# Optimization experiments

Measured on AMD Instinct MI355X. Metric: run time of the kernel, lower is better.

Reference implementation:

```python
import jax, jax.numpy as jnp
import numpy as np

B, T, OUT, IN, H = 128, 512, 256, 1024, 1024  # batch, seq_len, output_size, hidden_size(lstm in), input_size(lstm hidden)


def lstm_layer(x_seq, Wih, Whh, bih, bhh):
    """Single LSTM layer, PyTorch gate order (i, f, g, o).
    x_seq: [B, T, In] -> h_seq: [B, T, H]"""
    # input contribution is independent of the recurrence: compute once
    gx = jnp.einsum('bti,gi->btg', x_seq, Wih) + bih  # [B, T, 4H]
    gx = jnp.swapaxes(gx, 0, 1)  # [T, B, 4H] for scan over time
    Hh = Whh.shape[1]

    def step(carry, gxt):
        h, c = carry
        gates = gxt + h @ Whh.T + bhh  # [B, 4H]
        i, f, g, o = jnp.split(gates, 4, axis=-1)
        i = jax.nn.sigmoid(i)
        f = jax.nn.sigmoid(f)
        g = jnp.tanh(g)
        o = jax.nn.sigmoid(o)
        c = f * c + i * g
        h = o * jnp.tanh(c)
        return (h, c), h

    h0 = jnp.zeros((x_seq.shape[0], Hh), dtype=x_seq.dtype)
    c0 = jnp.zeros_like(h0)
    _, hs = jax.lax.scan(step, (h0, c0), gx)
    return jnp.swapaxes(hs, 0, 1)  # [B, T, H]


def setup_inputs() -> dict:
    key = jax.random.key(0)
    ks = jax.random.split(key, 12)
    s_fc = 1.0 / np.sqrt(OUT)
    s_l = 1.0 / np.sqrt(H)
    inp = {
        'x': jax.random.normal(ks[0], (B, OUT), dtype=jnp.float32),
        'fc_w': jax.random.uniform(ks[1], (IN, OUT), jnp.float32, -s_fc, s_fc),
        'fc_b': jax.random.uniform(ks[2], (IN,), jnp.float32, -s_fc, s_fc),
        'Wih0': jax.random.uniform(ks[3], (4 * H, IN), jnp.float32, -s_l, s_l),
        'Whh0': jax.random.uniform(ks[4], (4 * H, H), jnp.float32, -s_l, s_l),
        'bih0': jax.random.uniform(ks[5], (4 * H,), jnp.float32, -s_l, s_l),
        'bhh0': jax.random.uniform(ks[6], (4 * H,), jnp.float32, -s_l, s_l),
        'Wih1': jax.random.uniform(ks[7], (4 * H, H), jnp.float32, -s_l, s_l),
        'Whh1': jax.random.uniform(ks[8], (4 * H, H), jnp.float32, -s_l, s_l),
        'bih1': jax.random.uniform(ks[9], (4 * H,), jnp.float32, -s_l, s_l),
        'bhh1': jax.random.uniform(ks[10], (4 * H,), jnp.float32, -s_l, s_l),
    }
    return inp


def reference(x, fc_w, fc_b, Wih0, Whh0, bih0, bhh0, Wih1, Whh1, bih1, bhh1):
    # fc + (eval-mode) dropout, then broadcast the constant input across time
    z = x @ fc_w.T + fc_b  # [B, IN]
    z_seq = jnp.broadcast_to(z[:, None, :], (z.shape[0], T, z.shape[1]))  # [B, T, IN]
    h1 = lstm_layer(z_seq, Wih0, Whh0, bih0, bhh0)  # [B, T, H]
    # inter-layer dropout is identity in eval mode
    h2 = lstm_layer(h1, Wih1, Whh1, bih1, bhh1)  # [B, T, H]
    return h2
```

## Files before the change

kernel.cpp:

```cpp
#include <hip/hip_runtime.h>

typedef __attribute__((ext_vector_type(8))) short bf16x8;
typedef __attribute__((ext_vector_type(4))) float f32x4;
typedef unsigned short u16;
typedef unsigned long long u64;

#define T_SEQ 512
#define NBLK  192
#define FPAD  16
#define RSLOT 4

__device__ __forceinline__ u16 f2bf(float f) {
  unsigned int u = __float_as_uint(f);
  u += 0x7fffu + ((u >> 16) & 1u);
  return (u16)(u >> 16);
}
__device__ __forceinline__ float sigm_(float x) { return 1.f / (1.f + __expf(-x)); }
__device__ __forceinline__ float tanh_(float x) { return 1.f - 2.f / (__expf(2.f * x) + 1.f); }

template <typename T>
__device__ __forceinline__ void st_agent(T* p, T v) {
  __hip_atomic_store(p, v, __ATOMIC_RELAXED, __HIP_MEMORY_SCOPE_AGENT);
}
template <typename T>
__device__ __forceinline__ T ld_agent(const T* p) {
  return __hip_atomic_load(p, __ATOMIC_RELAXED, __HIP_MEMORY_SCOPE_AGENT);
}
__device__ __forceinline__ u64 pack2f(float a, float b) {
  return (u64)__float_as_uint(a) | ((u64)__float_as_uint(b) << 32);
}
__device__ __forceinline__ u64 pack4bf(f32x4 v) {
  return (u64)f2bf(v[0]) | ((u64)f2bf(v[1]) << 16) |
         ((u64)f2bf(v[2]) << 32) | ((u64)f2bf(v[3]) << 48);
}

__global__ void fc_kernel(const float* __restrict__ x, const float* __restrict__ w,
                          const float* __restrict__ bias, float* __restrict__ z) {
  int idx = blockIdx.x * 256 + threadIdx.x;
  int b = idx >> 10, i = idx & 1023;
  const float* xr = x + b * 256;
  const float* wr = w + i * 256;
  float acc = bias[i];
  #pragma unroll 4
  for (int o = 0; o < 256; ++o) acc += xr[o] * wr[o];
  z[idx] = acc;
}

__global__ void gx0_kernel(const float* __restrict__ z, const float* __restrict__ Wih0,
                           const float* __restrict__ bih, const float* __restrict__ bhh,
                           float* __restrict__ gx0) {
  int idx = blockIdx.x * 256 + threadIdx.x;
  int b = idx >> 12, j = idx & 4095;
  const float* zr = z + b * 1024;
  const float* wr = Wih0 + (size_t)j * 1024;
  float acc = bih[j] + bhh[j];
  #pragma unroll 4
  for (int k = 0; k < 1024; ++k) acc += zr[k] * wr[k];
  gx0[idx] = acc;
}

__global__ __launch_bounds__(512, 2)
void lstm_persist(const float* __restrict__ Whh0, const float* __restrict__ Wih1,
                  const float* __restrict__ Whh1, const float* __restrict__ gx0,
                  const float* __restrict__ bih1, const float* __restrict__ bhh1,
                  u16* __restrict__ h0ring, u16* __restrict__ h1ring,
                  float* __restrict__ pabuf, float* __restrict__ out,
                  int* __restrict__ h0flag, int* __restrict__ paflag,
                  int* __restrict__ h1flag) {
  __shared__ __align__(16) u16 wlds[4][2048][8];
  __shared__ __align__(16) float red[4][64][20];
  __shared__ __align__(16) float stage[128][20];

  const int bid = blockIdx.x;
  const int role = bid >> 6;
  const int cslice = bid & 63;
  const int cb = cslice * 16;
  const int tid = threadIdx.x;
  const int w = tid >> 6;
  const int lane = tid & 63;
  const int l15 = lane & 15;
  const int q = lane >> 4;
  const int Mg = w & 3;
  const int kh = w >> 2;

  {
    const float* Wsrc = (role == 0) ? Whh0 : (role == 1) ? Wih1 : Whh1;
    const int r = tid >> 3;
    const int g = r >> 4, n = r & 15;
    const int k0 = (tid & 7) * 128;
    const float* src = Wsrc + (((size_t)(g * 1024 + cb + n)) << 10) + k0;
    for (int k = 0; k < 128; k += 4) {
      float4 v = *(const float4*)(src + k);
      ushort4 o;
      o.x = f2bf(v.x); o.y = f2bf(v.y); o.z = f2bf(v.z); o.w = f2bf(v.w);
      const int kk = k0 + k;
      *(ushort4*)&wlds[g][((kk >> 3) << 4) + n][kk & 7] = o;
    }
  }

  float c_st[2][4];
  #pragma unroll
  for (int mt = 0; mt < 2; ++mt)
    #pragma unroll
    for (int r = 0; r < 4; ++r) c_st[mt][r] = 0.f;

  float gx[2][4][4];
  float b1[4];
  if (role == 0 && w < 4) {
    #pragma unroll
    for (int mt = 0; mt < 2; ++mt)
      #pragma unroll
      for (int g = 0; g < 4; ++g)
        #pragma unroll
        for (int r = 0; r < 4; ++r)
          gx[mt][g][r] = gx0[(size_t)(w * 32 + mt * 16 + q * 4 + r) * 4096 + g * 1024 + cb + l15];
  }
  if (role == 2 && w < 4) {
    #pragma unroll
    for (int g = 0; g < 4; ++g)
      b1[g] = bih1[g * 1024 + cb + l15] + bhh1[g * 1024 + cb + l15];
  }
  __syncthreads();

  const size_t HSLOT = (size_t)128 * 1024;

  for (int t = 0; t < T_SEQ; ++t) {
    const int sA = (t + 3) & 3;
    const int sW = t & 3;

    if (w == 0) {
      bool ok;
      if (role == 0) {
        do {
          int fa = ld_agent(h0flag + (sA * 64 + lane) * FPAD);
          int fb = ld_agent(paflag + (sW * 64 + lane) * FPAD);
          ok = __all(fa >= t && fb >= t - 3);
          if (!ok) __builtin_amdgcn_s_sleep(1);
        } while (!ok);
      } else if (role == 1) {
        do {
          int fa = ld_agent(h0flag + (sW * 64 + lane) * FPAD);
          int fb = (lane == 0) ? ld_agent(h1flag + (sW * 64 + cslice) * FPAD)
                               : 0x7fffffff;
          ok = __all(fa >= t + 1 && fb >= t - 3);
          if (!ok) __builtin_amdgcn_s_sleep(1);
        } while (!ok);
      } else {
        do {
          int fa = ld_agent(h1flag + (sA * 64 + lane) * FPAD);
          int fb = (lane == 0) ? ld_agent(paflag + (sW * 64 + cslice) * FPAD)
                               : 0x7fffffff;
          ok = __all(fa >= t && fb >= t + 1);
          if (!ok) __builtin_amdgcn_s_sleep(1);
        } while (!ok);
      }
      __builtin_amdgcn_fence(__ATOMIC_ACQUIRE, "agent");
    }
    __syncthreads();

    const u16* A = (role == 0) ? h0ring + (size_t)sA * HSLOT
                 : (role == 1) ? h0ring + (size_t)sW * HSLOT
                               : h1ring + (size_t)sA * HSLOT;

    const int kbase = kh * 512;
    const u16* Ap = A + (((size_t)(Mg * 32 + l15)) << 10) + kbase + q * 8;
    const int cellbase = ((kbase >> 3) + q) * 16 + l15;

    f32x4 acc0[4] = {{0.f,0.f,0.f,0.f},{0.f,0.f,0.f,0.f},{0.f,0.f,0.f,0.f},{0.f,0.f,0.f,0.f}};
    f32x4 acc1[4] = {{0.f,0.f,0.f,0.f},{0.f,0.f,0.f,0.f},{0.f,0.f,0.f,0.f},{0.f,0.f,0.f,0.f}};

    #pragma unroll
    for (int kk = 0; kk < 16; ++kk) {
      bf16x8 a0 = *(const bf16x8*)(Ap + kk * 32);
      bf16x8 a1 = *(const bf16x8*)(Ap + (16 << 10) + kk * 32);
      #pragma unroll
      for (int g = 0; g < 4; ++g) {
        bf16x8 b = *(const bf16x8*)&wlds[g][cellbase + kk * 64][0];
        acc0[g] = __builtin_amdgcn_mfma_f32_16x16x32_bf16(a0, b, acc0[g], 0, 0, 0);
        acc1[g] = __builtin_amdgcn_mfma_f32_16x16x32_bf16(a1, b, acc1[g], 0, 0, 0);
      }
    }

    u64 pa64[16];
    const float* pr = pabuf + (size_t)sW * 524288 + (size_t)(cslice * 4 + w) * 2048;
    if (role == 2 && w < 4) {
      #pragma unroll
      for (int j = 0; j < 8; ++j) {
        pa64[j * 2]     = ld_agent((const u64*)pr + j * 128 + lane * 2);
        pa64[j * 2 + 1] = ld_agent((const u64*)pr + j * 128 + lane * 2 + 1);
      }
    }

    if (w >= 4) {
      #pragma unroll
      for (int g = 0; g < 4; ++g) *(f32x4*)&red[w - 4][lane][g * 4] = acc0[g];
    }
    __syncthreads();
    if (w < 4) {
      #pragma unroll
      for (int g = 0; g < 4; ++g) acc0[g] += *(const f32x4*)&red[w][lane][g * 4];
    }
    __syncthreads();
    if (w >= 4) {
      #pragma unroll
      for (int g = 0; g < 4; ++g) *(f32x4*)&red[w - 4][lane][g * 4] = acc1[g];
    }
    __syncthreads();
    if (w < 4) {
      #pragma unroll
      for (int g = 0; g < 4; ++g) acc1[g] += *(const f32x4*)&red[w][lane][g * 4];

      if (role == 1) {
        float* pw = pabuf + (size_t)sW * 524288 + (size_t)(cslice * 4 + w) * 2048;
        #pragma unroll
        for (int g = 0; g < 4; ++g) {
          st_agent((u64*)pw + g * 128 + lane * 2,           pack2f(acc0[g][0], acc0[g][1]));
          st_agent((u64*)pw + g * 128 + lane * 2 + 1,       pack2f(acc0[g][2], acc0[g][3]));
          st_agent((u64*)pw + (4 + g) * 128 + lane * 2,     pack2f(acc1[g][0], acc1[g][1]));
          st_agent((u64*)pw + (4 + g) * 128 + lane * 2 + 1, pack2f(acc1[g][2], acc1[g][3]));
        }
      } else {
        #pragma unroll
        for (int mt = 0; mt < 2; ++mt) {
          #pragma unroll
          for (int r = 0; r < 4; ++r) {
            float xi, xf, xg, xo;
            f32x4* a = mt ? acc1 : acc0;
            if (role == 0) {
              xi = a[0][r] + gx[mt][0][r];
              xf = a[1][r] + gx[mt][1][r];
              xg = a[2][r] + gx[mt][2][r];
              xo = a[3][r] + gx[mt][3][r];
            } else {
              const int h2 = r >> 1, lo = r & 1;
              auto up = [&](int j) {
                u64 v = pa64[j * 2 + h2];
                return __uint_as_float(lo ? (unsigned)(v >> 32) : (unsigned)v);
              };
              xi = a[0][r] + up(mt * 4 + 0) + b1[0];
              xf = a[1][r] + up(mt * 4 + 1) + b1[1];
              xg = a[2][r] + up(mt * 4 + 2) + b1[2];
              xo = a[3][r] + up(mt * 4 + 3) + b1[3];
            }
            float i_ = sigm_(xi), f_ = sigm_(xf), g_ = tanh_(xg), o_ = sigm_(xo);
            float cn = f_ * c_st[mt][r] + i_ * g_;
            c_st[mt][r] = cn;
            float h = o_ * tanh_(cn);
            stage[w * 32 + mt * 16 + q * 4 + r][l15] = h;
          }
        }
      }
    }

    if (role != 1) {
      __syncthreads();
      const int row = tid >> 2, qt = tid & 3;
      f32x4 v = *(const f32x4*)&stage[row][qt * 4];
      u64 pk = pack4bf(v);
      if (role == 0) {
        st_agent((u64*)(h0ring + (size_t)sW * HSLOT + ((size_t)row << 10) + cb) + qt, pk);
      } else {
        st_agent((u64*)(h1ring + (size_t)sW * HSLOT + ((size_t)row << 10) + cb) + qt, pk);
        *(f32x4*)(out + (size_t)row * ((size_t)T_SEQ * 1024) + (size_t)t * 1024 + cb + qt * 4) = v;
      }
    }

    __syncthreads();
    if (tid == 0) {
      if (role == 0)      st_agent(h0flag + (sW * 64 + cslice) * FPAD, t + 1);
      else if (role == 1) st_agent(paflag + (sW * 64 + cslice) * FPAD, t + 1);
      else                st_agent(h1flag + (sW * 64 + cslice) * FPAD, t + 1);
    }
  }
}

extern "C" void kernel_launch(void* const* d_in, const int* in_sizes, int n_in,
                              void* d_out, int out_size, void* d_ws, size_t ws_size,
                              hipStream_t stream) {
  (void)in_sizes; (void)n_in; (void)out_size; (void)ws_size;
  const float* x    = (const float*)d_in[0];
  const float* fc_w = (const float*)d_in[1];
  const float* fc_b = (const float*)d_in[2];
  const float* Wih0 = (const float*)d_in[3];
  const float* Whh0 = (const float*)d_in[4];
  const float* bih0 = (const float*)d_in[5];
  const float* bhh0 = (const float*)d_in[6];
  const float* Wih1 = (const float*)d_in[7];
  const float* Whh1 = (const float*)d_in[8];
  const float* bih1 = (const float*)d_in[9];
  const float* bhh1 = (const float*)d_in[10];
  float* out = (float*)d_out;

  char* ws = (char*)d_ws;
  size_t off = 0;
  auto alloc = [&](size_t bytes) -> void* {
    void* p = ws + off;
    off += (bytes + 255) & ~(size_t)255;
    return p;
  };
  float* z      = (float*)alloc((size_t)128 * 1024 * 4);
  float* gx0    = (float*)alloc((size_t)128 * 4096 * 4);
  u16*   h0ring = (u16*)alloc((size_t)RSLOT * 128 * 1024 * 2);
  u16*   h1ring = (u16*)alloc((size_t)RSLOT * 128 * 1024 * 2);
  float* pabuf  = (float*)alloc((size_t)RSLOT * 524288 * 4);
  int*   h0flag = (int*)alloc((size_t)RSLOT * 64 * FPAD * 4);
  int*   paflag = (int*)alloc((size_t)RSLOT * 64 * FPAD * 4);
  int*   h1flag = (int*)alloc((size_t)RSLOT * 64 * FPAD * 4);

  hipMemsetAsync(h0ring, 0, (size_t)RSLOT * 128 * 1024 * 2, stream);
  hipMemsetAsync(h1ring, 0, (size_t)RSLOT * 128 * 1024 * 2, stream);
  hipMemsetAsync(h0flag, 0, (size_t)RSLOT * 64 * FPAD * 4, stream);
  hipMemsetAsync(paflag, 0, (size_t)RSLOT * 64 * FPAD * 4, stream);
  hipMemsetAsync(h1flag, 0, (size_t)RSLOT * 64 * FPAD * 4, stream);

  fc_kernel<<<512, 256, 0, stream>>>(x, fc_w, fc_b, z);
  gx0_kernel<<<2048, 256, 0, stream>>>(z, Wih0, bih0, bhh0, gx0);

  lstm_persist<<<NBLK, 512, 0, stream>>>(Whh0, Wih1, Whh1, gx0, bih1, bhh1,
                                         h0ring, h1ring, pabuf, out,
                                         h0flag, paflag, h1flag);
}
```

Baseline: 6.998 ms.

## Keep half the weights in registers and decentralize per-wave flag polling

Two of the four gate weight slices now live in VGPRs as bf16 fragments, and only the other two stay in LDS, which cuts per-step LDS reads. Each wave now polls only the producer flags covering its own K half instead of one wave polling all of them before a block barrier. The secondary dependency waits (pabuf readiness, ring-slot reuse) move to the points where they are actually needed. Flags become a single monotonic counter per slice instead of per-slot arrays, and the two-phase reduction merges into one with a wider scratch buffer. This removes barriers and LDS traffic from the serial recurrence, but raises register pressure under the 512x2 launch bounds, which risks spills.

```diff
diff --git a/kernel.cpp b/kernel.cpp
--- a/kernel.cpp
+++ b/kernel.cpp
@@ -67,8 +67,8 @@
                   float* __restrict__ pabuf, float* __restrict__ out,
                   int* __restrict__ h0flag, int* __restrict__ paflag,
                   int* __restrict__ h1flag) {
-  __shared__ __align__(16) u16 wlds[4][2048][8];
-  __shared__ __align__(16) float red[4][64][20];
+  __shared__ __align__(16) u16 wlds2[2][2048][8];
+  __shared__ __align__(16) float red[4][64][44];
   __shared__ __align__(16) float stage[128][20];
 
   const int bid = blockIdx.x;
@@ -83,18 +83,38 @@
   const int Mg = w & 3;
   const int kh = w >> 2;
 
+  const float* Wsrc = (role == 0) ? Whh0 : (role == 1) ? Wih1 : Whh1;
+
   {
-    const float* Wsrc = (role == 0) ? Whh0 : (role == 1) ? Wih1 : Whh1;
-    const int r = tid >> 3;
-    const int g = r >> 4, n = r & 15;
-    const int k0 = (tid & 7) * 128;
-    const float* src = Wsrc + (((size_t)(g * 1024 + cb + n)) << 10) + k0;
-    for (int k = 0; k < 128; k += 4) {
+    const int r = tid >> 4;
+    const int g2 = r >> 4, n = r & 15;
+    const int k0 = (tid & 15) * 64;
+    const float* src = Wsrc + (((size_t)((2 + g2) * 1024 + cb + n)) << 10) + k0;
+    for (int k = 0; k < 64; k += 4) {
       float4 v = *(const float4*)(src + k);
       ushort4 o;
       o.x = f2bf(v.x); o.y = f2bf(v.y); o.z = f2bf(v.z); o.w = f2bf(v.w);
       const int kk = k0 + k;
-      *(ushort4*)&wlds[g][((kk >> 3) << 4) + n][kk & 7] = o;
+      *(ushort4*)&wlds2[g2][((kk >> 3) << 4) + n][kk & 7] = o;
+    }
+  }
+
+  bf16x8 breg[2][16];
+  {
+    #pragma unroll
+    for (int g = 0; g < 2; ++g) {
+      const float* wrow = Wsrc + (((size_t)(g * 1024 + cb + l15)) << 10) + kh * 512 + q * 8;
+      #pragma unroll
+      for (int kk = 0; kk < 16; ++kk) {
+        float4 v0 = *(const float4*)(wrow + kk * 32);
+        float4 v1 = *(const float4*)(wrow + kk * 32 + 4);
+        union { bf16x8 v; u16 u[8]; } tmp;
+        tmp.u[0] = f2bf(v0.x); tmp.u[1] = f2bf(v0.y);
+        tmp.u[2] = f2bf(v0.z); tmp.u[3] = f2bf(v0.w);
+        tmp.u[4] = f2bf(v1.x); tmp.u[5] = f2bf(v1.y);
+        tmp.u[6] = f2bf(v1.z); tmp.u[7] = f2bf(v1.w);
+        breg[g][kk] = tmp.v;
+      }
     }
   }
 
@@ -128,35 +148,18 @@
     const int sA = (t + 3) & 3;
     const int sW = t & 3;
 
-    if (w == 0) {
+    {
+      const int pl = kh * 32 + (lane & 31);
+      const int* fl = (role == 2) ? h1flag : h0flag;
+      const int thr = (role == 1) ? t + 1 : t;
       bool ok;
-      if (role == 0) {
-        do {
-          int fa = ld_agent(h0flag + (sA * 64 + lane) * FPAD);
-          int fb = ld_agent(paflag + (sW * 64 + lane) * FPAD);
-          ok = __all(fa >= t && fb >= t - 3);
-          if (!ok) __builtin_amdgcn_s_sleep(1);
-        } while (!ok);
-      } else if (role == 1) {
-        do {
-          int fa = ld_agent(h0flag + (sW * 64 + lane) * FPAD);
-          int fb = (lane == 0) ? ld_agent(h1flag + (sW * 64 + cslice) * FPAD)
-                               : 0x7fffffff;
-          ok = __all(fa >= t + 1 && fb >= t - 3);
-          if (!ok) __builtin_amdgcn_s_sleep(1);
-        } while (!ok);
-      } else {
-        do {
-          int fa = ld_agent(h1flag + (sA * 64 + lane) * FPAD);
-          int fb = (lane == 0) ? ld_agent(paflag + (sW * 64 + cslice) * FPAD)
-                               : 0x7fffffff;
-          ok = __all(fa >= t && fb >= t + 1);
-          if (!ok) __builtin_amdgcn_s_sleep(1);
-        } while (!ok);
-      }
+      do {
+        int f = ld_agent(fl + pl * FPAD);
+        ok = __all(f >= thr);
+        if (!ok) __builtin_amdgcn_s_sleep(1);
+      } while (!ok);
       __builtin_amdgcn_fence(__ATOMIC_ACQUIRE, "agent");
     }
-    __syncthreads();
 
     const u16* A = (role == 0) ? h0ring + (size_t)sA * HSLOT
                  : (role == 1) ? h0ring + (size_t)sW * HSLOT
@@ -173,17 +176,22 @@
     for (int kk = 0; kk < 16; ++kk) {
       bf16x8 a0 = *(const bf16x8*)(Ap + kk * 32);
       bf16x8 a1 = *(const bf16x8*)(Ap + (16 << 10) + kk * 32);
-      #pragma unroll
-      for (int g = 0; g < 4; ++g) {
-        bf16x8 b = *(const bf16x8*)&wlds[g][cellbase + kk * 64][0];
-        acc0[g] = __builtin_amdgcn_mfma_f32_16x16x32_bf16(a0, b, acc0[g], 0, 0, 0);
-        acc1[g] = __builtin_amdgcn_mfma_f32_16x16x32_bf16(a1, b, acc1[g], 0, 0, 0);
-      }
+      acc0[0] = __builtin_amdgcn_mfma_f32_16x16x32_bf16(a0, breg[0][kk], acc0[0], 0, 0, 0);
+      acc1[0] = __builtin_amdgcn_mfma_f32_16x16x32_bf16(a1, breg[0][kk], acc1[0], 0, 0, 0);
+      acc0[1] = __builtin_amdgcn_mfma_f32_16x16x32_bf16(a0, breg[1][kk], acc0[1], 0, 0, 0);
+      acc1[1] = __builtin_amdgcn_mfma_f32_16x16x32_bf16(a1, breg[1][kk], acc1[1], 0, 0, 0);
+      bf16x8 b2 = *(const bf16x8*)&wlds2[0][cellbase + kk * 64][0];
+      acc0[2] = __builtin_amdgcn_mfma_f32_16x16x32_bf16(a0, b2, acc0[2], 0, 0, 0);
+      acc1[2] = __builtin_amdgcn_mfma_f32_16x16x32_bf16(a1, b2, acc1[2], 0, 0, 0);
+      bf16x8 b3 = *(const bf16x8*)&wlds2[1][cellbase + kk * 64][0];
+      acc0[3] = __builtin_amdgcn_mfma_f32_16x16x32_bf16(a0, b3, acc0[3], 0, 0, 0);
+      acc1[3] = __builtin_amdgcn_mfma_f32_16x16x32_bf16(a1, b3, acc1[3], 0, 0, 0);
     }
 
     u64 pa64[16];
     const float* pr = pabuf + (size_t)sW * 524288 + (size_t)(cslice * 4 + w) * 2048;
     if (role == 2 && w < 4) {
+      while (ld_agent(paflag + cslice * FPAD) < t + 1) __builtin_amdgcn_s_sleep(1);
       #pragma unroll
       for (int j = 0; j < 8; ++j) {
         pa64[j * 2]     = ld_agent((const u64*)pr + j * 128 + lane * 2);
@@ -193,24 +201,21 @@
 
     if (w >= 4) {
       #pragma unroll
-      for (int g = 0; g < 4; ++g) *(f32x4*)&red[w - 4][lane][g * 4] = acc0[g];
+      for (int g = 0; g < 4; ++g) {
+        *(f32x4*)&red[w - 4][lane][g * 4]      = acc0[g];
+        *(f32x4*)&red[w - 4][lane][16 + g * 4] = acc1[g];
+      }
     }
     __syncthreads();
     if (w < 4) {
       #pragma unroll
-      for (int g = 0; g < 4; ++g) acc0[g] += *(const f32x4*)&red[w][lane][g * 4];
-    }
-    __syncthreads();
-    if (w >= 4) {
-      #pragma unroll
-      for (int g = 0; g < 4; ++g) *(f32x4*)&red[w - 4][lane][g * 4] = acc1[g];
-    }
-    __syncthreads();
-    if (w < 4) {
-      #pragma unroll
-      for (int g = 0; g < 4; ++g) acc1[g] += *(const f32x4*)&red[w][lane][g * 4];
+      for (int g = 0; g < 4; ++g) {
+        acc0[g] += *(const f32x4*)&red[w][lane][g * 4];
+        acc1[g] += *(const f32x4*)&red[w][lane][16 + g * 4];
+      }
 
       if (role == 1) {
+        while (ld_agent(h1flag + cslice * FPAD) < t - 3) __builtin_amdgcn_s_sleep(1);
         float* pw = pabuf + (size_t)sW * 524288 + (size_t)(cslice * 4 + w) * 2048;
         #pragma unroll
         for (int g = 0; g < 4; ++g) {
@@ -254,6 +259,14 @@
 
     if (role != 1) {
       __syncthreads();
+      if (role == 0) {
+        bool ok;
+        do {
+          int f = ld_agent(paflag + lane * FPAD);
+          ok = __all(f >= t - 3);
+          if (!ok) __builtin_amdgcn_s_sleep(1);
+        } while (!ok);
+      }
       const int row = tid >> 2, qt = tid & 3;
       f32x4 v = *(const f32x4*)&stage[row][qt * 4];
       u64 pk = pack4bf(v);
@@ -261,15 +274,18 @@
         st_agent((u64*)(h0ring + (size_t)sW * HSLOT + ((size_t)row << 10) + cb) + qt, pk);
       } else {
         st_agent((u64*)(h1ring + (size_t)sW * HSLOT + ((size_t)row << 10) + cb) + qt, pk);
+      }
+      __syncthreads();
+      if (tid == 0) {
+        if (role == 0) st_agent(h0flag + cslice * FPAD, t + 1);
+        else           st_agent(h1flag + cslice * FPAD, t + 1);
+      }
+      if (role == 2) {
         *(f32x4*)(out + (size_t)row * ((size_t)T_SEQ * 1024) + (size_t)t * 1024 + cb + qt * 4) = v;
       }
-    }
-
-    __syncthreads();
-    if (tid == 0) {
-      if (role == 0)      st_agent(h0flag + (sW * 64 + cslice) * FPAD, t + 1);
-      else if (role == 1) st_agent(paflag + (sW * 64 + cslice) * FPAD, t + 1);
-      else                st_agent(h1flag + (sW * 64 + cslice) * FPAD, t + 1);
+    } else {
+      __syncthreads();
+      if (tid == 0) st_agent(paflag + cslice * FPAD, t + 1);
     }
   }
 }
@@ -303,15 +319,15 @@
   u16*   h0ring = (u16*)alloc((size_t)RSLOT * 128 * 1024 * 2);
   u16*   h1ring = (u16*)alloc((size_t)RSLOT * 128 * 1024 * 2);
   float* pabuf  = (float*)alloc((size_t)RSLOT * 524288 * 4);
-  int*   h0flag = (int*)alloc((size_t)RSLOT * 64 * FPAD * 4);
-  int*   paflag = (int*)alloc((size_t)RSLOT * 64 * FPAD * 4);
-  int*   h1flag = (int*)alloc((size_t)RSLOT * 64 * FPAD * 4);
+  int*   h0flag = (int*)alloc((size_t)64 * FPAD * 4);
+  int*   paflag = (int*)alloc((size_t)64 * FPAD * 4);
+  int*   h1flag = (int*)alloc((size_t)64 * FPAD * 4);
 
   hipMemsetAsync(h0ring, 0, (size_t)RSLOT * 128 * 1024 * 2, stream);
   hipMemsetAsync(h1ring, 0, (size_t)RSLOT * 128 * 1024 * 2, stream);
-  hipMemsetAsync(h0flag, 0, (size_t)RSLOT * 64 * FPAD * 4, stream);
-  hipMemsetAsync(paflag, 0, (size_t)RSLOT * 64 * FPAD * 4, stream);
-  hipMemsetAsync(h1flag, 0, (size_t)RSLOT * 64 * FPAD * 4, stream);
+  hipMemsetAsync(h0flag, 0, (size_t)64 * FPAD * 4, stream);
+  hipMemsetAsync(paflag, 0, (size_t)64 * FPAD * 4, stream);
+  hipMemsetAsync(h1flag, 0, (size_t)64 * FPAD * 4, stream);
 
   fc_kernel<<<512, 256, 0, stream>>>(x, fc_w, fc_b, z);
   gx0_kernel<<<2048, 256, 0, stream>>>(z, Wih0, bih0, bhh0, gx0);
```

New measurement: 12.51 ms. +78.8%, slower.

## Split inter-block flag waits per wave and defer ring-slot reuse checks

Applied to the files above, without the earlier changes.

Replaces the single wave-0 spin plus block barrier with every wave polling only the producer flags for its own K-half. Secondary waits (pabuf readiness, ring-slot reuse) move to the point right before the data is consumed or overwritten. Flags collapse from per-slot arrays to one monotonic counter per column slice. The aim is to shorten the serial critical path of the per-timestep handoff between layer-0, projection and layer-1 blocks. The cost is more polling traffic from all waves and subtler ordering invariants that could race.

```diff
diff --git a/kernel.cpp b/kernel.cpp
--- a/kernel.cpp
+++ b/kernel.cpp
@@ -128,35 +128,18 @@
     const int sA = (t + 3) & 3;
     const int sW = t & 3;
 
-    if (w == 0) {
+    {
+      const int pl = kh * 32 + (lane & 31);
+      const int* fl = (role == 2) ? h1flag : h0flag;
+      const int thr = (role == 1) ? t + 1 : t;
       bool ok;
-      if (role == 0) {
-        do {
-          int fa = ld_agent(h0flag + (sA * 64 + lane) * FPAD);
-          int fb = ld_agent(paflag + (sW * 64 + lane) * FPAD);
-          ok = __all(fa >= t && fb >= t - 3);
-          if (!ok) __builtin_amdgcn_s_sleep(1);
-        } while (!ok);
-      } else if (role == 1) {
-        do {
-          int fa = ld_agent(h0flag + (sW * 64 + lane) * FPAD);
-          int fb = (lane == 0) ? ld_agent(h1flag + (sW * 64 + cslice) * FPAD)
-                               : 0x7fffffff;
-          ok = __all(fa >= t + 1 && fb >= t - 3);
-          if (!ok) __builtin_amdgcn_s_sleep(1);
-        } while (!ok);
-      } else {
-        do {
-          int fa = ld_agent(h1flag + (sA * 64 + lane) * FPAD);
-          int fb = (lane == 0) ? ld_agent(paflag + (sW * 64 + cslice) * FPAD)
-                               : 0x7fffffff;
-          ok = __all(fa >= t && fb >= t + 1);
-          if (!ok) __builtin_amdgcn_s_sleep(1);
-        } while (!ok);
-      }
+      do {
+        int f = ld_agent(fl + pl * FPAD);
+        ok = __all(f >= thr);
+        if (!ok) __builtin_amdgcn_s_sleep(1);
+      } while (!ok);
       __builtin_amdgcn_fence(__ATOMIC_ACQUIRE, "agent");
     }
-    __syncthreads();
 
     const u16* A = (role == 0) ? h0ring + (size_t)sA * HSLOT
                  : (role == 1) ? h0ring + (size_t)sW * HSLOT
@@ -184,6 +167,7 @@
     u64 pa64[16];
     const float* pr = pabuf + (size_t)sW * 524288 + (size_t)(cslice * 4 + w) * 2048;
     if (role == 2 && w < 4) {
+      while (ld_agent(paflag + cslice * FPAD) < t + 1) __builtin_amdgcn_s_sleep(1);
       #pragma unroll
       for (int j = 0; j < 8; ++j) {
         pa64[j * 2]     = ld_agent((const u64*)pr + j * 128 + lane * 2);
@@ -211,6 +195,7 @@
       for (int g = 0; g < 4; ++g) acc1[g] += *(const f32x4*)&red[w][lane][g * 4];
 
       if (role == 1) {
+        while (ld_agent(h1flag + cslice * FPAD) < t - 3) __builtin_amdgcn_s_sleep(1);
         float* pw = pabuf + (size_t)sW * 524288 + (size_t)(cslice * 4 + w) * 2048;
         #pragma unroll
         for (int g = 0; g < 4; ++g) {
@@ -254,6 +239,14 @@
 
     if (role != 1) {
       __syncthreads();
+      if (role == 0) {
+        bool ok;
+        do {
+          int f = ld_agent(paflag + lane * FPAD);
+          ok = __all(f >= t - 3);
+          if (!ok) __builtin_amdgcn_s_sleep(1);
+        } while (!ok);
+      }
       const int row = tid >> 2, qt = tid & 3;
       f32x4 v = *(const f32x4*)&stage[row][qt * 4];
       u64 pk = pack4bf(v);
@@ -261,15 +254,18 @@
         st_agent((u64*)(h0ring + (size_t)sW * HSLOT + ((size_t)row << 10) + cb) + qt, pk);
       } else {
         st_agent((u64*)(h1ring + (size_t)sW * HSLOT + ((size_t)row << 10) + cb) + qt, pk);
+      }
+      __syncthreads();
+      if (tid == 0) {
+        if (role == 0) st_agent(h0flag + cslice * FPAD, t + 1);
+        else           st_agent(h1flag + cslice * FPAD, t + 1);
+      }
+      if (role == 2) {
         *(f32x4*)(out + (size_t)row * ((size_t)T_SEQ * 1024) + (size_t)t * 1024 + cb + qt * 4) = v;
       }
-    }
-
-    __syncthreads();
-    if (tid == 0) {
-      if (role == 0)      st_agent(h0flag + (sW * 64 + cslice) * FPAD, t + 1);
-      else if (role == 1) st_agent(paflag + (sW * 64 + cslice) * FPAD, t + 1);
-      else                st_agent(h1flag + (sW * 64 + cslice) * FPAD, t + 1);
+    } else {
+      __syncthreads();
+      if (tid == 0) st_agent(paflag + cslice * FPAD, t + 1);
     }
   }
 }
@@ -303,15 +299,15 @@
   u16*   h0ring = (u16*)alloc((size_t)RSLOT * 128 * 1024 * 2);
   u16*   h1ring = (u16*)alloc((size_t)RSLOT * 128 * 1024 * 2);
   float* pabuf  = (float*)alloc((size_t)RSLOT * 524288 * 4);
-  int*   h0flag = (int*)alloc((size_t)RSLOT * 64 * FPAD * 4);
-  int*   paflag = (int*)alloc((size_t)RSLOT * 64 * FPAD * 4);
-  int*   h1flag = (int*)alloc((size_t)RSLOT * 64 * FPAD * 4);
+  int*   h0flag = (int*)alloc((size_t)64 * FPAD * 4);
+  int*   paflag = (int*)alloc((size_t)64 * FPAD * 4);
+  int*   h1flag = (int*)alloc((size_t)64 * FPAD * 4);
 
   hipMemsetAsync(h0ring, 0, (size_t)RSLOT * 128 * 1024 * 2, stream);
   hipMemsetAsync(h1ring, 0, (size_t)RSLOT * 128 * 1024 * 2, stream);
-  hipMemsetAsync(h0flag, 0, (size_t)RSLOT * 64 * FPAD * 4, stream);
-  hipMemsetAsync(paflag, 0, (size_t)RSLOT * 64 * FPAD * 4, stream);
-  hipMemsetAsync(h1flag, 0, (size_t)RSLOT * 64 * FPAD * 4, stream);
+  hipMemsetAsync(h0flag, 0, (size_t)64 * FPAD * 4, stream);
+  hipMemsetAsync(paflag, 0, (size_t)64 * FPAD * 4, stream);
+  hipMemsetAsync(h1flag, 0, (size_t)64 * FPAD * 4, stream);
 
   fc_kernel<<<512, 256, 0, stream>>>(x, fc_w, fc_b, z);
   gx0_kernel<<<2048, 256, 0, stream>>>(z, Wih0, bih0, bhh0, gx0);
```

Result: slower. 11.13 ms (+59.0%).
